# Kernel tuning notes

Measured on AMD Instinct MI355X. Metric: run time of the kernel, lower is better.

The kernel has to match this reference:

```python
import jax, jax.numpy as jnp
import numpy as np

N_HEADS, D_MODEL, D_HEAD = 16, 1024, 64
INIT_STD = 0.02
IGNORE = -100000.0


def setup_inputs() -> dict:
    key = jax.random.key(0)
    ks = jax.random.split(key, 5)
    x = jax.random.normal(ks[0], (2, 2048, D_MODEL), dtype=jnp.float32)
    W_Q = INIT_STD * jax.random.normal(ks[1], (N_HEADS, D_MODEL, D_HEAD), dtype=jnp.float32)
    W_K = INIT_STD * jax.random.normal(ks[2], (N_HEADS, D_MODEL, D_HEAD), dtype=jnp.float32)
    W_V = INIT_STD * jax.random.normal(ks[3], (N_HEADS, D_MODEL, D_HEAD), dtype=jnp.float32)
    W_O = INIT_STD * jax.random.normal(ks[4], (N_HEADS, D_HEAD, D_MODEL), dtype=jnp.float32)
    b_Q = jnp.zeros((N_HEADS, D_HEAD), dtype=jnp.float32)
    b_K = jnp.zeros((N_HEADS, D_HEAD), dtype=jnp.float32)
    b_V = jnp.zeros((N_HEADS, D_HEAD), dtype=jnp.float32)
    b_O = jnp.zeros((D_MODEL,), dtype=jnp.float32)
    return {"normalized_resid_pre": x, "W_Q": W_Q, "W_K": W_K, "W_V": W_V,
            "W_O": W_O, "b_Q": b_Q, "b_K": b_K, "b_V": b_V, "b_O": b_O}


def reference(normalized_resid_pre, W_Q, W_K, W_V, W_O, b_Q, b_K, b_V, b_O):
    x = normalized_resid_pre  # [b, s, d_model]
    q = jnp.einsum('bsm,hmd->bshd', x, W_Q) + b_Q  # [b, s, h, d_head]
    k = jnp.einsum('bsm,hmd->bshd', x, W_K) + b_K
    v = jnp.einsum('bsm,hmd->bshd', x, W_V) + b_V
    scores = jnp.einsum('bqhd,bkhd->bhqk', q, k) / jnp.sqrt(jnp.float32(D_HEAD))
    s = x.shape[1]
    causal = jnp.triu(jnp.ones((s, s), dtype=bool), k=1)  # True above diagonal
    scores = jnp.where(causal, jnp.float32(IGNORE), scores)
    pattern = jax.nn.softmax(scores, axis=-1)  # [b, h, q, k]
    z = jnp.einsum('bkhd,bhqk->bqhd', v, pattern)
    attn_out = jnp.einsum('bqhd,hdm->bqm', z, W_O) + b_O
    return attn_out
```

## Files before the change

kernel.cpp:

```cpp
#include <hip/hip_runtime.h>
#include <hip/hip_bf16.h>

#define BB   2
#define SS   2048
#define HH   16
#define DM_  1024
#define DH_  64
#define NROW 4096
#define NQKV 3072

typedef unsigned short u16;
typedef unsigned int u32;
using short4v = __attribute__((ext_vector_type(4))) short;
using short8 = __attribute__((ext_vector_type(8))) short;
using bf16x8 = __attribute__((ext_vector_type(8))) __bf16;
using f32x4  = __attribute__((ext_vector_type(4))) float;
using f32x16 = __attribute__((ext_vector_type(16))) float;

#define QSCALE 0.180336880f

__device__ __forceinline__ u16 f2bf(float f) {
    union { float f; unsigned u; } v; v.f = f;
    unsigned r = v.u + 0x7fffu + ((v.u >> 16) & 1u);
    return (u16)(r >> 16);
}

__device__ __forceinline__ f32x4 mfma16(bf16x8 a, bf16x8 b, f32x4 c) {
    return __builtin_amdgcn_mfma_f32_16x16x32_bf16(a, b, c, 0, 0, 0);
}
__device__ __forceinline__ f32x16 mfma32(bf16x8 a, bf16x8 b, f32x16 c) {
    return __builtin_amdgcn_mfma_f32_32x32x16_bf16(a, b, c, 0, 0, 0);
}

__device__ __forceinline__ u32 cvtpk(float lo, float hi) {
    u32 r;
    asm("v_cvt_pk_bf16_f32 %0, %1, %2" : "=v"(r) : "v"(lo), "v"(hi));
    return r;
}
#define PLSWAP(a, b) asm("v_permlane32_swap_b32 %0, %1" : "+v"(a), "+v"(b))

__device__ __forceinline__ float fexp2(float x) {
#if __has_builtin(__builtin_amdgcn_exp2f)
    return __builtin_amdgcn_exp2f(x);
#else
    float r; asm("v_exp_f32 %0, %1" : "=v"(r) : "v"(x)); return r;
#endif
}

__device__ __forceinline__ void gload16(const void* g, void* l) {
    __builtin_amdgcn_global_load_lds(
        (const __attribute__((address_space(1))) void*)g,
        (__attribute__((address_space(3))) void*)l, 16, 0, 0);
}

__global__ __launch_bounds__(256)
void prep(const float* __restrict__ x,  const float* __restrict__ wq,
          const float* __restrict__ wk, const float* __restrict__ wv,
          const float* __restrict__ wo, const float* __restrict__ bq,
          const float* __restrict__ bk, const float* __restrict__ bv,
          u16* __restrict__ Xb, u16* __restrict__ Wt,
          u16* __restrict__ WoT, float* __restrict__ biasQKV) {
    __shared__ float tile[64][65];
    const int bx = blockIdx.x, t = threadIdx.x;
    if (bx < 512) {
        const int tid = bx * 256 + t;
        #pragma unroll
        for (int it = 0; it < 8; ++it) {
            int i = tid + it * 131072;
            float4 v = ((const float4*)x)[i];
            u16 b4[4] = {f2bf(v.x), f2bf(v.y), f2bf(v.z), f2bf(v.w)};
            ((short4v*)Xb)[i] = *(short4v*)b4;
        }
        if (tid < NQKV) {
            int mat = tid >> 10, h = (tid >> 6) & 15, d = tid & 63;
            const float* bb = (mat == 0) ? bq : ((mat == 1) ? bk : bv);
            biasQKV[tid] = bb[h * DH_ + d];
        }
    } else if (bx < 1280) {
        const int idx = bx - 512;
        const int m0 = (idx & 15) * 64, hm = idx >> 4;
        const int mat = hm >> 4, h = hm & 15;
        const float* w = (mat == 0) ? wq : ((mat == 1) ? wk : wv);
        #pragma unroll
        for (int it = 0; it < 4; ++it) {
            int row = it * 16 + (t >> 4), c4 = (t & 15) * 4;
            float4 v = *(const float4*)&w[((size_t)h * 1024 + m0 + row) * 64 + c4];
            tile[row][c4] = v.x; tile[row][c4 + 1] = v.y;
            tile[row][c4 + 2] = v.z; tile[row][c4 + 3] = v.w;
        }
        __syncthreads();
        #pragma unroll
        for (int it = 0; it < 2; ++it) {
            int c = it * 256 + t, d = c >> 3, mc = (c & 7) * 8;
            u16 buf[8];
            #pragma unroll
            for (int j = 0; j < 8; ++j) buf[j] = f2bf(tile[mc + j][d]);
            *(short8*)&Wt[((size_t)(mat * 1024 + h * 64 + d)) * 1024 + m0 + mc] = *(short8*)buf;
        }
    } else {
        const int idx = bx - 1280;
        const int n0 = (idx & 15) * 64, k0 = (idx >> 4) * 64;
        #pragma unroll
        for (int it = 0; it < 4; ++it) {
            int row = it * 16 + (t >> 4), c4 = (t & 15) * 4;
            float4 v = *(const float4*)&wo[(size_t)(k0 + row) * DM_ + n0 + c4];
            tile[row][c4] = v.x; tile[row][c4 + 1] = v.y;
            tile[row][c4 + 2] = v.z; tile[row][c4 + 3] = v.w;
        }
        __syncthreads();
        #pragma unroll
        for (int it = 0; it < 2; ++it) {
            int c = it * 256 + t, n = c >> 3, kc = (c & 7) * 8;
            u16 buf[8];
            #pragma unroll
            for (int j = 0; j < 8; ++j) buf[j] = f2bf(tile[kc + j][n]);
            *(short8*)&WoT[(size_t)(n0 + n) * DM_ + k0 + kc] = *(short8*)buf;
        }
    }
}

__device__ __forceinline__ void gemm_core_128(
    const u16* __restrict__ Ap, const u16* __restrict__ Bp,
    int brow, int bcol, u16* lds, f32x4 acc[4][2]) {
    const int t = threadIdx.x, l = t & 63;
    const int wid = t >> 6, wm = wid >> 2, wn = wid & 3;
    const int c0 = t, c1 = t + 512;
    const int r0 = c0 >> 3, sb0 = ((c0 & 7) ^ (r0 & 7)) << 3;
    const int r1 = c1 >> 3, sb1 = ((c1 & 7) ^ (r1 & 7)) << 3;
    u16* A0 = lds;
    u16* B0 = lds + 16384;
    const int rA0 = wm * 64 + (l & 15);
    const int rB0 = wn * 32 + (l & 15);
    const int sw  = (l & 7) << 3;
    const int colA = ((l >> 4) << 3);

    {
        gload16(Ap + (size_t)(brow + r0) * DM_ + sb0, A0 + c0 * 8);
        gload16(Ap + (size_t)(brow + r1) * DM_ + sb1, A0 + c1 * 8);
        gload16(Bp + (size_t)(bcol + r0) * DM_ + sb0, B0 + c0 * 8);
        gload16(Bp + (size_t)(bcol + r1) * DM_ + sb1, B0 + c1 * 8);
    }
    __syncthreads();
    for (int kt = 0; kt < 16; ++kt) {
        const int p = kt & 1;
        if (kt < 15) {
            const int ko = (kt + 1) * 64;
            gload16(Ap + (size_t)(brow + r0) * DM_ + ko + sb0, A0 + (p ^ 1) * 8192 + c0 * 8);
            gload16(Ap + (size_t)(brow + r1) * DM_ + ko + sb1, A0 + (p ^ 1) * 8192 + c1 * 8);
            gload16(Bp + (size_t)(bcol + r0) * DM_ + ko + sb0, B0 + (p ^ 1) * 8192 + c0 * 8);
            gload16(Bp + (size_t)(bcol + r1) * DM_ + ko + sb1, B0 + (p ^ 1) * 8192 + c1 * 8);
        }
        const u16* Ab = A0 + p * 8192;
        const u16* Bb = B0 + p * 8192;
        #pragma unroll
        for (int kc = 0; kc < 64; kc += 32) {
            const int cx = (kc + colA) ^ sw;
            bf16x8 af[4], bfr[2];
            #pragma unroll
            for (int m = 0; m < 4; ++m)
                af[m] = *(const bf16x8*)(Ab + (rA0 + m * 16) * 64 + cx);
            #pragma unroll
            for (int n = 0; n < 2; ++n)
                bfr[n] = *(const bf16x8*)(Bb + (rB0 + n * 16) * 64 + cx);
            __builtin_amdgcn_s_setprio(1);
            #pragma unroll
            for (int m = 0; m < 4; ++m)
                #pragma unroll
                for (int n = 0; n < 2; ++n)
                    acc[m][n] = mfma16(af[m], bfr[n], acc[m][n]);
            __builtin_amdgcn_s_setprio(0);
        }
        __syncthreads();
    }
}

__global__ __launch_bounds__(512)
void gemm_qkv3(const u16* __restrict__ Xb, const u16* __restrict__ Wt,
               const float* __restrict__ bias, u16* __restrict__ Qs,
               u16* __restrict__ Ks, u16* __restrict__ Vt) {
    __shared__ __align__(16) u16 lds[32768];
    const int bx = blockIdx.x, t = threadIdx.x, l = t & 63;
    const int wid = t >> 6, wm = wid >> 2, wn = wid & 3;
    f32x4 acc[4][2] = {};
    const bool isV = (bx >= 512);
    int brow, bcol; const u16 *Ap, *Bp;
    if (!isV) { brow = (bx & 31) * 128; bcol = (bx >> 5) * 128; Ap = Xb; Bp = Wt; }
    else { int i2 = bx - 512; brow = (i2 & 7) * 128; bcol = (i2 >> 3) * 128;
           Ap = Wt + (size_t)2048 * DM_; Bp = Xb; }
    gemm_core_128(Ap, Bp, brow, bcol, lds, acc);

    u16* wr_ = lds + wid * 2048;
    const int colbase = bcol + wn * 32;
    const int rowbase = brow + wm * 64;
    const int rsub = ((l >> 4) << 2);
    if (!isV) {
        const float b0 = bias[colbase + (l & 15)];
        const float b1 = bias[colbase + 16 + (l & 15)];
        const float scl = (colbase < 1024) ? QSCALE : 1.0f;
        #pragma unroll
        for (int m = 0; m < 4; ++m)
            #pragma unroll
            for (int n = 0; n < 2; ++n) {
                const float bb = n ? b1 : b0;
                #pragma unroll
                for (int r = 0; r < 4; ++r)
                    wr_[(m * 16 + rsub + r) * 32 + n * 16 + (l & 15)] =
                        f2bf((acc[m][n][r] + bb) * scl);
            }
    } else {
        #pragma unroll
        for (int m = 0; m < 4; ++m) {
            float4 bv = *(const float4*)&bias[2048 + rowbase + m * 16 + rsub];
            const float bbr[4] = {bv.x, bv.y, bv.z, bv.w};
            #pragma unroll
            for (int n = 0; n < 2; ++n)
                #pragma unroll
                for (int r = 0; r < 4; ++r)
                    wr_[(m * 16 + rsub + r) * 32 + n * 16 + (l & 15)] =
                        f2bf(acc[m][n][r] + bbr[r]);
        }
    }
    __syncthreads();
    if (!isV) {
        const int hsel = (colbase >> 6) & 15, d0 = colbase & 63;
        const int bsel = rowbase >> 11, s0 = rowbase & 2047;
        u16* outp = (colbase < 1024) ? Qs : Ks;
        #pragma unroll
        for (int p = 0; p < 4; ++p) {
            const int rr = p * 16 + (l >> 2);
            short8 v = *(const short8*)(wr_ + rr * 32 + (l & 3) * 8);
            *(short8*)&outp[(((size_t)bsel * HH + hsel) * SS + s0 + rr) * DH_ + d0 + (l & 3) * 8] = v;
        }
    } else {
        const int bsel = colbase >> 11, s0 = colbase & 2047;
        #pragma unroll
        for (int p = 0; p < 4; ++p) {
            const int rr = p * 16 + (l >> 2);
            short8 v = *(const short8*)(wr_ + rr * 32 + (l & 3) * 8);
            *(short8*)&Vt[((size_t)bsel * 1024 + rowbase + rr) * SS + s0 + (l & 3) * 8] = v;
        }
    }
}

__global__ __launch_bounds__(512)
void gemm_out3(const u16* __restrict__ Zb, const u16* __restrict__ WoT,
               const float* __restrict__ bO, float* __restrict__ out) {
    __shared__ __align__(16) u16 lds[32768];
    const int bx = blockIdx.x, t = threadIdx.x, l = t & 63;
    const int wid = t >> 6, wm = wid >> 2, wn = wid & 3;
    const int brow = (bx & 31) * 128, bcol = (bx >> 5) * 128;
    f32x4 acc[4][2] = {};
    gemm_core_128(Zb, WoT, brow, bcol, lds, acc);
    const int colbase = bcol + wn * 32;
    const int rowbase = brow + wm * 64;
    const int rsub = ((l >> 4) << 2);
    const float b0 = bO[colbase + (l & 15)];
    const float b1 = bO[colbase + 16 + (l & 15)];
    #pragma unroll
    for (int m = 0; m < 4; ++m)
        #pragma unroll
        for (int n = 0; n < 2; ++n) {
            const float bb = n ? b1 : b0;
            #pragma unroll
            for (int r = 0; r < 4; ++r)
                out[(size_t)(rowbase + m * 16 + rsub + r) * DM_ + colbase + n * 16 + (l & 15)] =
                    acc[m][n][r] + bb;
        }
}

__global__ __launch_bounds__(256, 4)
void attn_fwd(const u16* __restrict__ Qs, const u16* __restrict__ Ks,
              const u16* __restrict__ Vt, u16* __restrict__ Zb) {
    __shared__ __align__(16) u16 fKV[16384];
    __shared__ __align__(16) float lrP[64];
    __shared__ __align__(16) float lrX[64];
    const int bidx = blockIdx.x;
    const int j  = (bidx < 512) ? (31 - (bidx >> 5)) : ((bidx - 512) >> 5);
    const int bh = bidx & 31, b = bh >> 4, h = bh & 15;
    const int t = threadIdx.x, wid = t >> 6, l = t & 63;
    const int hi = l >> 5, c32 = l & 31;
    const int qh = wid >> 1, par = wid & 1, wp = qh;
    const u16* Qp = Qs + (size_t)bh * SS * DH_;
    const u16* Kp = Ks + (size_t)bh * SS * DH_;
    const u16* Vp = Vt + (size_t)bh * DH_ * SS;
    const int qw = j * 64 + qh * 32;
    const int nr = (j >> 1) + 1;

    bf16x8 aq[4];
    #pragma unroll
    for (int dk = 0; dk < 4; ++dk)
        aq[dk] = *(const bf16x8*)&Qp[(size_t)(qw + c32) * DH_ + dk * 16 + hi * 8];

    int kOff[2]; size_t vOff[2]; int dstc[2];
    #pragma unroll
    for (int i = 0; i < 2; ++i) {
        const int c = t + 256 * i, sec = c >> 6, ln = c & 63;
        kOff[i] = ((sec >> 2) * 32 + (ln & 31)) * DH_ + (sec & 3) * 16 + (ln >> 5) * 8;
        vOff[i] = (size_t)((sec >> 2) * 32 + (ln & 31)) * SS + (sec & 3) * 16 + (ln >> 5) * 8;
        dstc[i] = c * 8;
    }
    u16* fK0 = fKV;          u16* fK1 = fKV + 4096;
    u16* fV0 = fKV + 8192;   u16* fV1 = fKV + 12288;
    const u16* fKb = par ? fK1 : fK0;
    const u16* fVb = par ? fV1 : fV0;

    f32x16 o0 = {}, o1 = {};
    float lrp[4] = {0.f, 0.f, 0.f, 0.f};

    for (int r = 0; r < nr; ++r) {
        const int k0a = r * 128, k0b = r * 128 + 64;
        __syncthreads();
        #pragma unroll
        for (int i = 0; i < 2; ++i) {
            gload16(Kp + (size_t)k0a * DH_ + kOff[i], fK0 + dstc[i]);
            gload16(Kp + (size_t)k0b * DH_ + kOff[i], fK1 + dstc[i]);
            gload16(Vp + k0a + vOff[i], fV0 + dstc[i]);
            gload16(Vp + k0b + vOff[i], fV1 + dstc[i]);
        }
        __syncthreads();
        const int kv0 = r * 128 + par * 64;
        if (kv0 <= qw + 31) {
            const bool have1 = (kv0 + 32 <= qw + 31);
            f32x16 s0 = {}, s1 = {};
            __builtin_amdgcn_s_setprio(1);
            #pragma unroll
            for (int dk = 0; dk < 4; ++dk)
                s0 = mfma32(*(const bf16x8*)(fKb + dk * 512 + l * 8), aq[dk], s0);
            if (have1) {
                #pragma unroll
                for (int dk = 0; dk < 4; ++dk)
                    s1 = mfma32(*(const bf16x8*)(fKb + (4 + dk) * 512 + l * 8), aq[dk], s1);
            }
            __builtin_amdgcn_s_setprio(0);
            if (kv0 + 63 > qw) {
                const int q = qw + c32;
                #pragma unroll
                for (int r16 = 0; r16 < 16; ++r16) {
                    const int crow = (r16 & 3) + 8 * (r16 >> 2) + 4 * hi;
                    if (kv0 + crow > q) s0[r16] = -1e30f;
                }
                if (have1) {
                    #pragma unroll
                    for (int r16 = 0; r16 < 16; ++r16) {
                        const int crow = (r16 & 3) + 8 * (r16 >> 2) + 4 * hi;
                        if (kv0 + 32 + crow > q) s1[r16] = -1e30f;
                    }
                }
            }
            #pragma unroll
            for (int r16 = 0; r16 < 16; ++r16) {
                s0[r16] = fexp2(s0[r16]);
                lrp[r16 & 3] += s0[r16];
            }
            if (have1) {
                #pragma unroll
                for (int r16 = 0; r16 < 16; ++r16) {
                    s1[r16] = fexp2(s1[r16]);
                    lrp[r16 & 3] += s1[r16];
                }
            }
            __builtin_amdgcn_s_setprio(1);
            #define PV_STEP(PS, B8, KS)                                          \
            {                                                                    \
                u32 cA  = cvtpk(PS[B8 + 0], PS[B8 + 1]);                         \
                u32 cA2 = cvtpk(PS[B8 + 2], PS[B8 + 3]);                         \
                u32 cB  = cvtpk(PS[B8 + 4], PS[B8 + 5]);                         \
                u32 cB2 = cvtpk(PS[B8 + 6], PS[B8 + 7]);                         \
                PLSWAP(cA, cB); PLSWAP(cA2, cB2);                                \
                u32 w[4] = {cA, cA2, cB, cB2};                                   \
                bf16x8 pa = *(bf16x8*)w;                                         \
                o0 = mfma32(pa, *(const bf16x8*)(fVb + (0 * 4 + (KS)) * 512 + l * 8), o0); \
                o1 = mfma32(pa, *(const bf16x8*)(fVb + (1 * 4 + (KS)) * 512 + l * 8), o1); \
            }
            PV_STEP(s0, 0, 0)
            PV_STEP(s0, 8, 1)
            if (have1) {
                PV_STEP(s1, 0, 2)
                PV_STEP(s1, 8, 3)
            }
            #undef PV_STEP
            __builtin_amdgcn_s_setprio(0);
        }
    }
    float lrow = (lrp[0] + lrp[1]) + (lrp[2] + lrp[3]);
    lrow += __shfl_xor(lrow, 32);

    float* mrg = (float*)fKV;
    __syncthreads();
    if (par) {
        #pragma unroll
        for (int e = 0; e < 16; ++e) mrg[wp * 2048 + e * 64 + l] = o0[e];
        #pragma unroll
        for (int e = 0; e < 16; ++e) mrg[wp * 2048 + (16 + e) * 64 + l] = o1[e];
        if (hi == 0) lrP[wp * 32 + c32] = lrow;
    }
    __syncthreads();
    if (!par) {
        #pragma unroll
        for (int e = 0; e < 16; ++e) o0[e] += mrg[wp * 2048 + e * 64 + l];
        #pragma unroll
        for (int e = 0; e < 16; ++e) o1[e] += mrg[wp * 2048 + (16 + e) * 64 + l];
        lrow += lrP[wp * 32 + c32];
        lrX[wp * 32 + c32] = lrow;
        float invv[16];
        #pragma unroll
        for (int g = 0; g < 4; ++g) {
            float4 lv = *(const float4*)&lrX[wp * 32 + 8 * g + 4 * hi];
            invv[g * 4 + 0] = 1.0f / lv.x;
            invv[g * 4 + 1] = 1.0f / lv.y;
            invv[g * 4 + 2] = 1.0f / lv.z;
            invv[g * 4 + 3] = 1.0f / lv.w;
        }
        #pragma unroll
        for (int r16 = 0; r16 < 16; ++r16) {
            const int q = qw + (r16 & 3) + 8 * (r16 >> 2) + 4 * hi;
            u16* zp = &Zb[(((size_t)b * SS + q) * HH + h) * DH_];
            zp[c32]      = f2bf(o0[r16] * invv[r16]);
            zp[32 + c32] = f2bf(o1[r16] * invv[r16]);
        }
    }
}

extern "C" void kernel_launch(void* const* d_in, const int* in_sizes, int n_in,
                              void* d_out, int out_size, void* d_ws, size_t ws_size,
                              hipStream_t stream) {
    const float* x  = (const float*)d_in[0];
    const float* wq = (const float*)d_in[1];
    const float* wk = (const float*)d_in[2];
    const float* wv = (const float*)d_in[3];
    const float* wo = (const float*)d_in[4];
    const float* bq = (const float*)d_in[5];
    const float* bk = (const float*)d_in[6];
    const float* bv = (const float*)d_in[7];
    const float* bO = (const float*)d_in[8];
    float* out = (float*)d_out;

    char* w = (char*)d_ws;
    u16* Xb  = (u16*)w;  w += (size_t)NROW * DM_ * 2;
    u16* Wt  = (u16*)w;  w += (size_t)NQKV * DM_ * 2;
    u16* WoT = (u16*)w;  w += (size_t)DM_ * DM_ * 2;
    float* biasQKV = (float*)w; w += (size_t)NQKV * 4;
    u16* Qs  = (u16*)w;  w += (size_t)BB * HH * SS * DH_ * 2;
    u16* Ks  = (u16*)w;  w += (size_t)BB * HH * SS * DH_ * 2;
    u16* Vt  = (u16*)w;  w += (size_t)BB * HH * SS * DH_ * 2;
    u16* Zb  = (u16*)w;  w += (size_t)BB * HH * SS * DH_ * 2;

    prep<<<1536, 256, 0, stream>>>(x, wq, wk, wv, wo, bq, bk, bv,
                                   Xb, Wt, WoT, biasQKV);
    gemm_qkv3<<<768, 512, 0, stream>>>(Xb, Wt, biasQKV, Qs, Ks, Vt);
    attn_fwd<<<1024, 256, 0, stream>>>(Qs, Ks, Vt, Zb);
    gemm_out3<<<256, 512, 0, stream>>>(Zb, WoT, bO, out);
}
```

Baseline: 97.00 us.

## Prefetch next K/V tile into registers to overlap global loads with compute

Replaces the direct global-to-LDS loads at the top of each iteration with a register-staged software pipeline. Tile r+1 is already held in registers and is written to LDS after computing tile r, and then tile r+2 is loaded, so global latency overlaps the MFMA work. This raises VGPR pressure by eight short8 registers and gives up the async LDS-direct load path, which may hurt occupancy.

```diff
diff --git a/kernel.cpp b/kernel.cpp
--- a/kernel.cpp
+++ b/kernel.cpp
@@ -304,20 +304,34 @@
     const u16* fKb = par ? fK1 : fK0;
     const u16* fVb = par ? fV1 : fV0;
 
+    short8 sg0, sg1, sg2, sg3, sg4, sg5, sg6, sg7;
+    #define LOADR(rr)                                                        \
+    {   const int ka = (rr) * 128, kb2 = (rr) * 128 + 64;                    \
+        sg0 = *(const short8*)(Kp + (size_t)ka * DH_ + kOff[0]);             \
+        sg1 = *(const short8*)(Kp + (size_t)ka * DH_ + kOff[1]);             \
+        sg2 = *(const short8*)(Kp + (size_t)kb2 * DH_ + kOff[0]);            \
+        sg3 = *(const short8*)(Kp + (size_t)kb2 * DH_ + kOff[1]);            \
+        sg4 = *(const short8*)(Vp + ka + vOff[0]);                           \
+        sg5 = *(const short8*)(Vp + ka + vOff[1]);                           \
+        sg6 = *(const short8*)(Vp + kb2 + vOff[0]);                          \
+        sg7 = *(const short8*)(Vp + kb2 + vOff[1]);                          \
+    }
+    #define WRITER()                                                         \
+    {   *(short8*)(fK0 + dstc[0]) = sg0;  *(short8*)(fK0 + dstc[1]) = sg1;   \
+        *(short8*)(fK1 + dstc[0]) = sg2;  *(short8*)(fK1 + dstc[1]) = sg3;   \
+        *(short8*)(fV0 + dstc[0]) = sg4;  *(short8*)(fV0 + dstc[1]) = sg5;   \
+        *(short8*)(fV1 + dstc[0]) = sg6;  *(short8*)(fV1 + dstc[1]) = sg7;   \
+    }
+
+    LOADR(0)
+    WRITER()
+    LOADR(1)
+    __syncthreads();
+
     f32x16 o0 = {}, o1 = {};
     float lrp[4] = {0.f, 0.f, 0.f, 0.f};
 
     for (int r = 0; r < nr; ++r) {
-        const int k0a = r * 128, k0b = r * 128 + 64;
-        __syncthreads();
-        #pragma unroll
-        for (int i = 0; i < 2; ++i) {
-            gload16(Kp + (size_t)k0a * DH_ + kOff[i], fK0 + dstc[i]);
-            gload16(Kp + (size_t)k0b * DH_ + kOff[i], fK1 + dstc[i]);
-            gload16(Vp + k0a + vOff[i], fV0 + dstc[i]);
-            gload16(Vp + k0b + vOff[i], fV1 + dstc[i]);
-        }
-        __syncthreads();
         const int kv0 = r * 128 + par * 64;
         if (kv0 <= qw + 31) {
             const bool have1 = (kv0 + 32 <= qw + 31);
@@ -381,7 +395,16 @@
             #undef PV_STEP
             __builtin_amdgcn_s_setprio(0);
         }
-    }
+        __syncthreads();
+        if (r + 1 < nr) {
+            WRITER()
+            if (r + 2 < nr) LOADR(r + 2)
+            __syncthreads();
+        }
+    }
+    #undef LOADR
+    #undef WRITER
+
     float lrow = (lrp[0] + lrp[1]) + (lrp[2] + lrp[3]);
     lrow += __shfl_xor(lrow, 32);
 
```

After: 132.9 us. +37.0%, slower.

## Double-buffer K/V tiles and widen attention blocks to 128 queries

Applied to the files above, without the earlier changes.

The attention kernel now uses 512-thread blocks, each covering 128 queries (half as many blocks), and keeps two LDS buffers for K and V. While one 128-key tile is being consumed, the next tile's global-to-LDS loads are already issued, so each iteration has one barrier instead of two. This aims to hide K/V load latency behind the MFMA work and to reuse each loaded tile across more queries. The cost is twice the LDS per block (about 64KB), which limits how many blocks fit on a CU, plus a different causal load balance across blocks.

```diff
diff --git a/kernel.cpp b/kernel.cpp
--- a/kernel.cpp
+++ b/kernel.cpp
@@ -268,23 +268,24 @@
         }
 }
 
-__global__ __launch_bounds__(256, 4)
+__global__ __launch_bounds__(512, 4)
 void attn_fwd(const u16* __restrict__ Qs, const u16* __restrict__ Ks,
               const u16* __restrict__ Vt, u16* __restrict__ Zb) {
-    __shared__ __align__(16) u16 fKV[16384];
-    __shared__ __align__(16) float lrP[64];
-    __shared__ __align__(16) float lrX[64];
+    __shared__ __align__(16) u16 fK[2][8192];
+    __shared__ __align__(16) u16 fV[2][8192];
+    __shared__ float lrP[128];
+    __shared__ float lrX[128];
     const int bidx = blockIdx.x;
-    const int j  = (bidx < 512) ? (31 - (bidx >> 5)) : ((bidx - 512) >> 5);
+    const int j  = (bidx < 256) ? (15 - (bidx >> 5)) : ((bidx - 256) >> 5);
     const int bh = bidx & 31, b = bh >> 4, h = bh & 15;
     const int t = threadIdx.x, wid = t >> 6, l = t & 63;
     const int hi = l >> 5, c32 = l & 31;
-    const int qh = wid >> 1, par = wid & 1, wp = qh;
+    const int qh = wid >> 1, par = wid & 1;
     const u16* Qp = Qs + (size_t)bh * SS * DH_;
     const u16* Kp = Ks + (size_t)bh * SS * DH_;
     const u16* Vp = Vt + (size_t)bh * DH_ * SS;
-    const int qw = j * 64 + qh * 32;
-    const int nr = (j >> 1) + 1;
+    const int qw = j * 128 + qh * 32;
+    const int nr = j + 1;
 
     bf16x8 aq[4];
     #pragma unroll
@@ -294,32 +295,34 @@
     int kOff[2]; size_t vOff[2]; int dstc[2];
     #pragma unroll
     for (int i = 0; i < 2; ++i) {
-        const int c = t + 256 * i, sec = c >> 6, ln = c & 63;
-        kOff[i] = ((sec >> 2) * 32 + (ln & 31)) * DH_ + (sec & 3) * 16 + (ln >> 5) * 8;
-        vOff[i] = (size_t)((sec >> 2) * 32 + (ln & 31)) * SS + (sec & 3) * 16 + (ln >> 5) * 8;
+        const int c = t + 512 * i, sec = c >> 6, ln = c & 63;
+        const int kh = sec >> 3, s7 = sec & 7;
+        kOff[i] = (kh * 64 + (s7 >> 2) * 32 + (ln & 31)) * DH_ + (s7 & 3) * 16 + (ln >> 5) * 8;
+        vOff[i] = (size_t)((s7 >> 2) * 32 + (ln & 31)) * SS + kh * 64 + (s7 & 3) * 16 + (ln >> 5) * 8;
         dstc[i] = c * 8;
     }
-    u16* fK0 = fKV;          u16* fK1 = fKV + 4096;
-    u16* fV0 = fKV + 8192;   u16* fV1 = fKV + 12288;
-    const u16* fKb = par ? fK1 : fK0;
-    const u16* fVb = par ? fV1 : fV0;
+
+    #define ISSUE(rr, pb)                                                     \
+    {   const int ka = (rr) * 128;                                            \
+        gload16(Kp + (size_t)ka * DH_ + kOff[0], &fK[pb][dstc[0]]);           \
+        gload16(Kp + (size_t)ka * DH_ + kOff[1], &fK[pb][dstc[1]]);           \
+        gload16(Vp + ka + vOff[0], &fV[pb][dstc[0]]);                         \
+        gload16(Vp + ka + vOff[1], &fV[pb][dstc[1]]);                         \
+    }
+
+    ISSUE(0, 0)
+    __syncthreads();
 
     f32x16 o0 = {}, o1 = {};
     float lrp[4] = {0.f, 0.f, 0.f, 0.f};
 
     for (int r = 0; r < nr; ++r) {
-        const int k0a = r * 128, k0b = r * 128 + 64;
-        __syncthreads();
-        #pragma unroll
-        for (int i = 0; i < 2; ++i) {
-            gload16(Kp + (size_t)k0a * DH_ + kOff[i], fK0 + dstc[i]);
-            gload16(Kp + (size_t)k0b * DH_ + kOff[i], fK1 + dstc[i]);
-            gload16(Vp + k0a + vOff[i], fV0 + dstc[i]);
-            gload16(Vp + k0b + vOff[i], fV1 + dstc[i]);
-        }
-        __syncthreads();
+        const int p = r & 1;
+        if (r + 1 < nr) ISSUE(r + 1, p ^ 1)
         const int kv0 = r * 128 + par * 64;
         if (kv0 <= qw + 31) {
+            const u16* fKb = &fK[p][par * 4096];
+            const u16* fVb = &fV[p][par * 4096];
             const bool have1 = (kv0 + 32 <= qw + 31);
             f32x16 s0 = {}, s1 = {};
             __builtin_amdgcn_s_setprio(1);
@@ -381,31 +384,34 @@
             #undef PV_STEP
             __builtin_amdgcn_s_setprio(0);
         }
-    }
+        __syncthreads();
+    }
+    #undef ISSUE
+
     float lrow = (lrp[0] + lrp[1]) + (lrp[2] + lrp[3]);
     lrow += __shfl_xor(lrow, 32);
 
-    float* mrg = (float*)fKV;
+    float* mrg = (float*)fK;
     __syncthreads();
     if (par) {
         #pragma unroll
-        for (int e = 0; e < 16; ++e) mrg[wp * 2048 + e * 64 + l] = o0[e];
-        #pragma unroll
-        for (int e = 0; e < 16; ++e) mrg[wp * 2048 + (16 + e) * 64 + l] = o1[e];
-        if (hi == 0) lrP[wp * 32 + c32] = lrow;
+        for (int e = 0; e < 16; ++e) mrg[qh * 2048 + e * 64 + l] = o0[e];
+        #pragma unroll
+        for (int e = 0; e < 16; ++e) mrg[qh * 2048 + (16 + e) * 64 + l] = o1[e];
+        if (hi == 0) lrP[qh * 32 + c32] = lrow;
     }
     __syncthreads();
     if (!par) {
         #pragma unroll
-        for (int e = 0; e < 16; ++e) o0[e] += mrg[wp * 2048 + e * 64 + l];
-        #pragma unroll
-        for (int e = 0; e < 16; ++e) o1[e] += mrg[wp * 2048 + (16 + e) * 64 + l];
-        lrow += lrP[wp * 32 + c32];
-        lrX[wp * 32 + c32] = lrow;
+        for (int e = 0; e < 16; ++e) o0[e] += mrg[qh * 2048 + e * 64 + l];
+        #pragma unroll
+        for (int e = 0; e < 16; ++e) o1[e] += mrg[qh * 2048 + (16 + e) * 64 + l];
+        lrow += lrP[qh * 32 + c32];
+        lrX[qh * 32 + c32] = lrow;
         float invv[16];
         #pragma unroll
         for (int g = 0; g < 4; ++g) {
-            float4 lv = *(const float4*)&lrX[wp * 32 + 8 * g + 4 * hi];
+            float4 lv = *(const float4*)&lrX[qh * 32 + 8 * g + 4 * hi];
             invv[g * 4 + 0] = 1.0f / lv.x;
             invv[g * 4 + 1] = 1.0f / lv.y;
             invv[g * 4 + 2] = 1.0f / lv.z;
@@ -448,6 +454,6 @@
     prep<<<1536, 256, 0, stream>>>(x, wq, wk, wv, wo, bq, bk, bv,
                                    Xb, Wt, WoT, biasQKV);
     gemm_qkv3<<<768, 512, 0, stream>>>(Xb, Wt, biasQKV, Qs, Ks, Vt);
-    attn_fwd<<<1024, 256, 0, stream>>>(Qs, Ks, Vt, Zb);
+    attn_fwd<<<512, 512, 0, stream>>>(Qs, Ks, Vt, Zb);
     gemm_out3<<<256, 512, 0, stream>>>(Zb, WoT, bO, out);
 }
```

New measurement: 95.52 us. No clear change (-1.5%).
